# Kernel optimization log

Hardware: AMD Instinct MI355X
Metric: run time of the kernel (lower is better)

The kernel has to match this reference:

```python
import jax, jax.numpy as jnp
import numpy as np

N = 100000      # nodes
E = 1600000     # edges (before self-loops)
IN = 64         # in_channels
HID = 16        # hidden_channels
HEADS = 4       # num_heads
G = 512         # number of graphs in batch
SLOPE = 0.2     # GATConv leaky_relu negative_slope


def setup_inputs() -> dict:
    key = jax.random.key(0)
    ks = jax.random.split(key, 12)
    s = 0.1
    x = jax.random.normal(ks[0], (N, IN), jnp.float32)
    edge_index = jax.random.randint(ks[1], (2, E), 0, N, dtype=jnp.int64)
    batch = jnp.sort(jax.random.randint(ks[2], (N,), 0, G, dtype=jnp.int64))
    W1 = jax.random.normal(ks[3], (IN, HEADS * HID), jnp.float32) * s
    a1_src = jax.random.normal(ks[4], (HEADS, HID), jnp.float32) * s
    a1_dst = jax.random.normal(ks[5], (HEADS, HID), jnp.float32) * s
    b1 = jnp.zeros((HEADS * HID,), jnp.float32)
    W2 = jax.random.normal(ks[6], (HEADS * HID, HID), jnp.float32) * s
    a2_src = jax.random.normal(ks[7], (1, HID), jnp.float32) * s
    a2_dst = jax.random.normal(ks[8], (1, HID), jnp.float32) * s
    b2 = jnp.zeros((HID,), jnp.float32)
    Wc = jax.random.normal(ks[9], (HID, 1), jnp.float32) * s
    bc = jnp.zeros((1,), jnp.float32)
    return dict(x=x, edge_index=edge_index, batch=batch, W1=W1, a1_src=a1_src,
                a1_dst=a1_dst, b1=b1, W2=W2, a2_src=a2_src, a2_dst=a2_dst,
                b2=b2, Wc=Wc, bc=bc)


def gat_layer(x, src, dst, W, a_s, a_d, bias, heads, out_ch, concat):
    # PyG GATConv: linear -> per-edge attention logits -> segment softmax over dst -> scatter aggregate
    n = x.shape[0]
    h = (x @ W).reshape(n, heads, out_ch)              # [N, H, C]
    al_s = jnp.sum(h * a_s, axis=-1)                   # [N, H]
    al_d = jnp.sum(h * a_d, axis=-1)                   # [N, H]
    e = al_s[src] + al_d[dst]                          # [E, H]
    e = jnp.where(e > 0, e, SLOPE * e)                 # leaky_relu
    m = jax.ops.segment_max(e, dst, num_segments=n)    # per-dst max (self-loops ensure non-empty)
    p = jnp.exp(e - m[dst])
    denom = jax.ops.segment_sum(p, dst, num_segments=n)
    alpha = p / (denom[dst] + 1e-16)                   # [E, H]
    out = jax.ops.segment_sum(h[src] * alpha[:, :, None], dst, num_segments=n)  # [N, H, C]
    out = out.reshape(n, heads * out_ch) if concat else out.mean(axis=1)
    return out + bias


def reference(x, edge_index, batch, W1, a1_src, a1_dst, b1, W2, a2_src, a2_dst, b2, Wc, bc):
    loops = jnp.arange(N, dtype=edge_index.dtype)      # GATConv add_self_loops=True
    src = jnp.concatenate([edge_index[0], loops])
    dst = jnp.concatenate([edge_index[1], loops])
    h = jax.nn.elu(gat_layer(x, src, dst, W1, a1_src, a1_dst, b1, HEADS, HID, True))
    # dropout inactive (eval mode)
    h = jax.nn.elu(gat_layer(h, src, dst, W2, a2_src, a2_dst, b2, 1, HID, False))
    counts = jax.ops.segment_sum(jnp.ones((N,), h.dtype), batch, num_segments=G)
    pooled = jax.ops.segment_sum(h, batch, num_segments=G) / jnp.maximum(counts, 1.0)[:, None]
    return pooled @ Wc + bc
```

## Files before the change

### kernel.cpp

```cpp
#include <hip/hip_runtime.h>
#include <hip/hip_fp16.h>
#include <hip/hip_fp8.h>

#define N_NODES 100000
#define N_EDGES 1600000
#define ET      (N_EDGES + N_NODES)
#define NG      512
#define SLOPE   0.2f

#define BKT_SHIFT 9
#define NB_B   ((N_NODES + 511) / 512)
#define BCAP   10240
#define CHUNK_A 8192
#define NBLK_A ((ET + CHUNK_A - 1) / CHUNK_A)
#define H1B4   ((N_NODES + 1023) / 1024)

typedef _Float16 half8_t __attribute__((ext_vector_type(8)));
typedef float    f32x4_t __attribute__((ext_vector_type(4)));

__global__ __launch_bounds__(1024) void k_prepA(
    const float* __restrict__ x, const float* __restrict__ W1,
    const float* __restrict__ a1s, const float* __restrict__ a1d,
    const int* __restrict__ ei,
    int* __restrict__ gcnt, unsigned int* __restrict__ ebuf,
    __hip_fp8_e4m3* __restrict__ h1, float* __restrict__ al1s, float* __restrict__ al1d)
{
    __shared__ union U {
        struct { float Wl[64 * 64]; float asf[64]; float adf[64]; } p;
        struct { unsigned int stage[CHUNK_A]; unsigned char sbin[CHUNK_A];
                 int hist[NB_B]; int binst[NB_B]; int resv[NB_B]; int cur[NB_B];
                 int tmp[1024]; } a;
    } u;
    int tid = threadIdx.x;

    if (blockIdx.x < NBLK_A) {
        int base = blockIdx.x * CHUNK_A;
        int m = min(CHUNK_A, ET - base);
        for (int i = tid; i < NB_B; i += 1024) u.a.hist[i] = 0;
        __syncthreads();
        for (int i = tid; i < m; i += 1024) {
            int eid = base + i;
            int d = (eid < N_EDGES) ? ei[N_EDGES + eid] : (eid - N_EDGES);
            atomicAdd(&u.a.hist[d >> BKT_SHIFT], 1);
        }
        __syncthreads();
        int v = (tid < NB_B) ? u.a.hist[tid] : 0;
        u.a.tmp[tid] = v;
        __syncthreads();
        for (int off = 1; off < 1024; off <<= 1) {
            int t = (tid >= off) ? u.a.tmp[tid - off] : 0;
            __syncthreads();
            u.a.tmp[tid] += t;
            __syncthreads();
        }
        if (tid < NB_B) {
            int e = u.a.tmp[tid] - v;
            u.a.binst[tid] = e;
            u.a.cur[tid] = e;
            u.a.resv[tid] = v ? atomicAdd(&gcnt[tid], v) : 0;
        }
        __syncthreads();
        for (int i = tid; i < m; i += 1024) {
            int eid = base + i;
            int s, d;
            if (eid < N_EDGES) { s = ei[eid]; d = ei[N_EDGES + eid]; }
            else               { s = eid - N_EDGES; d = s; }
            int b = d >> BKT_SHIFT;
            int pos = atomicAdd(&u.a.cur[b], 1);
            u.a.stage[pos] = ((unsigned int)(d & 511) << 17) | (unsigned int)s;
            u.a.sbin[pos] = (unsigned char)b;
        }
        __syncthreads();
        for (int i = tid; i < m; i += 1024) {
            int b = u.a.sbin[i];
            ebuf[b * BCAP + u.a.resv[b] + (i - u.a.binst[b])] = u.a.stage[i];
        }
        return;
    }

    for (int i = tid; i < 64 * 64; i += 1024) u.p.Wl[i] = W1[i];
    if (tid < 64) { u.p.asf[tid] = a1s[tid]; u.p.adf[tid] = a1d[tid]; }
    __syncthreads();

    int wv = tid >> 6, lane = tid & 63;
    int m = lane & 15, q = lane >> 4;

    half8_t bf[4][2];
#pragma unroll
    for (int t = 0; t < 4; ++t)
#pragma unroll
        for (int s = 0; s < 2; ++s) {
            half8_t b;
#pragma unroll
            for (int j = 0; j < 8; ++j)
                b[j] = (_Float16)u.p.Wl[(s * 32 + q * 8 + j) * 64 + t * 16 + m];
            bf[t][s] = b;
        }

    int nodebase = (blockIdx.x - NBLK_A) * 1024 + wv * 64;
    for (int it = 0; it < 4; ++it) {
        int node0 = nodebase + it * 16;
        int node = node0 + m;
        half8_t av0 = {}, av1 = {};
        if (node < N_NODES) {
            const float4* xr = (const float4*)(x + (long long)node * 64);
            float4 p0 = xr[q * 2], p1 = xr[q * 2 + 1];
            float4 p2 = xr[q * 2 + 8], p3 = xr[q * 2 + 9];
            av0[0] = (_Float16)p0.x; av0[1] = (_Float16)p0.y;
            av0[2] = (_Float16)p0.z; av0[3] = (_Float16)p0.w;
            av0[4] = (_Float16)p1.x; av0[5] = (_Float16)p1.y;
            av0[6] = (_Float16)p1.z; av0[7] = (_Float16)p1.w;
            av1[0] = (_Float16)p2.x; av1[1] = (_Float16)p2.y;
            av1[2] = (_Float16)p2.z; av1[3] = (_Float16)p2.w;
            av1[4] = (_Float16)p3.x; av1[5] = (_Float16)p3.y;
            av1[6] = (_Float16)p3.z; av1[7] = (_Float16)p3.w;
        }
        f32x4_t acc[4] = {{0,0,0,0},{0,0,0,0},{0,0,0,0},{0,0,0,0}};
#pragma unroll
        for (int t = 0; t < 4; ++t) {
            acc[t] = __builtin_amdgcn_mfma_f32_16x16x32_f16(av0, bf[t][0], acc[t], 0, 0, 0);
            acc[t] = __builtin_amdgcn_mfma_f32_16x16x32_f16(av1, bf[t][1], acc[t], 0, 0, 0);
        }
#pragma unroll
        for (int r = 0; r < 4; ++r) {
            int nr = node0 + q * 4 + r;
            bool ok = nr < N_NODES;
#pragma unroll
            for (int t = 0; t < 4; ++t) {
                float v = acc[t][r];
                if (ok) h1[(long long)nr * 64 + t * 16 + m] = __hip_fp8_e4m3(v);
                float ps = v * u.p.asf[t * 16 + m];
                float pd = v * u.p.adf[t * 16 + m];
                ps += __shfl_xor(ps, 1); ps += __shfl_xor(ps, 2);
                ps += __shfl_xor(ps, 4); ps += __shfl_xor(ps, 8);
                pd += __shfl_xor(pd, 1); pd += __shfl_xor(pd, 2);
                pd += __shfl_xor(pd, 4); pd += __shfl_xor(pd, 8);
                if (ok && m == t) { al1s[nr * 4 + t] = ps; al1d[nr * 4 + t] = pd; }
            }
        }
    }
}

__global__ __launch_bounds__(1024) void k_passB(
    const unsigned int* __restrict__ ebuf, const int* __restrict__ gcnt,
    int* __restrict__ csr, int* __restrict__ offs, int* __restrict__ deg)
{
    __shared__ int ldeg[512];
    __shared__ int lofs[512];
    __shared__ int lcur[512];
    int tid = threadIdx.x;
    int b = blockIdx.x;
    int nb0 = b << BKT_SHIFT;
    int nn = min(512, N_NODES - nb0);
    int gbase = b * BCAP, cnt = gcnt[b];
    if (tid < 512) ldeg[tid] = 0;
    __syncthreads();
    for (int i = tid; i < cnt; i += 1024)
        atomicAdd(&ldeg[ebuf[gbase + i] >> 17], 1);
    __syncthreads();
    int v = 0;
    if (tid < 512) { v = ldeg[tid]; lofs[tid] = v; }
    __syncthreads();
    for (int off = 1; off < 512; off <<= 1) {
        int t = (tid >= off && tid < 512) ? lofs[tid - off] : 0;
        __syncthreads();
        if (tid < 512) lofs[tid] += t;
        __syncthreads();
    }
    if (tid < 512) {
        int e = lofs[tid] - v;
        lcur[tid] = e;
        if (tid < nn) { offs[nb0 + tid] = gbase + e; deg[nb0 + tid] = v; }
    }
    __syncthreads();
    for (int i = tid; i < cnt; i += 1024) {
        unsigned int ev = ebuf[gbase + i];
        int dl = ev >> 17, s = (int)(ev & 0x1FFFF);
        int p = atomicAdd(&lcur[dl], 1);
        csr[gbase + p] = s;
    }
}

__global__ __launch_bounds__(256) void k_agg1(
    const int* __restrict__ offs, const int* __restrict__ deg, const int* __restrict__ csr,
    const __hip_fp8_e4m3* __restrict__ h1, const float* __restrict__ al1s, const float* __restrict__ al1d,
    const float* __restrict__ b1, __half* __restrict__ h1bg)
{
    __shared__ int   sarr[4][64];
    __shared__ float warr[4][4 * 72];
    __shared__ __align__(16) float h1b[4][64];
    int tid = threadIdx.x;
    int wv = tid >> 6, lane = tid & 63;
    int eslot = lane >> 4;
    int cq = lane & 15;
    int h = cq >> 2;
    int cq4 = cq * 4;
    int node = blockIdx.x * 4 + wv;
    int st = offs[node], dg = deg[node];
    const float4 ald4 = *(const float4*)(al1d + node * 4);
    float b1l = b1[lane];
    const char* __restrict__ h1c = (const char*)h1;

    float a0 = 0.f, a1 = 0.f, a2 = 0.f, a3 = 0.f, den = 0.f;
    for (int base = 0; base < dg; base += 64) {
        int m = min(64, dg - base);
        int s = 0;
        float w0 = 0.f, w1 = 0.f, w2 = 0.f, w3 = 0.f;
        if (lane < m) {
            s = csr[st + base + lane];
            const float4 as4 = *(const float4*)(al1s + s * 4);
            float e0 = as4.x + ald4.x; e0 = e0 > 0.f ? e0 : SLOPE * e0;
            float e1 = as4.y + ald4.y; e1 = e1 > 0.f ? e1 : SLOPE * e1;
            float e2 = as4.z + ald4.z; e2 = e2 > 0.f ? e2 : SLOPE * e2;
            float e3 = as4.w + ald4.w; e3 = e3 > 0.f ? e3 : SLOPE * e3;
            w0 = __expf(e0); w1 = __expf(e1); w2 = __expf(e2); w3 = __expf(e3);
        }
        sarr[wv][lane] = s << 6;
        warr[wv][0 * 72 + lane] = w0;
        warr[wv][1 * 72 + lane] = w1;
        warr[wv][2 * 72 + lane] = w2;
        warr[wv][3 * 72 + lane] = w3;
        int m4 = (m + 3) & ~3;
#pragma unroll 4
        for (int j0 = 0; j0 < m4; j0 += 4) {
            int j = j0 + eslot;
            int off = sarr[wv][j] + cq4;
            float wgt = warr[wv][h * 72 + j];
            unsigned int pk = *(const unsigned int*)(h1c + off);
            a0 = fmaf(wgt, __builtin_amdgcn_cvt_f32_fp8(pk, 0), a0);
            a1 = fmaf(wgt, __builtin_amdgcn_cvt_f32_fp8(pk, 1), a1);
            a2 = fmaf(wgt, __builtin_amdgcn_cvt_f32_fp8(pk, 2), a2);
            a3 = fmaf(wgt, __builtin_amdgcn_cvt_f32_fp8(pk, 3), a3);
            den += wgt;
        }
    }
    a0 += __shfl_xor(a0, 16); a0 += __shfl_xor(a0, 32);
    a1 += __shfl_xor(a1, 16); a1 += __shfl_xor(a1, 32);
    a2 += __shfl_xor(a2, 16); a2 += __shfl_xor(a2, 32);
    a3 += __shfl_xor(a3, 16); a3 += __shfl_xor(a3, 32);
    den += __shfl_xor(den, 16); den += __shfl_xor(den, 32);
    if (lane < 16)
        *(float4*)&h1b[wv][cq4] = make_float4(a0, a1, a2, a3);
    float denc = __shfl(den, (lane >> 4) << 2);
    float v = h1b[wv][lane] / (denc + 1e-16f) + b1l;
    v = v > 0.f ? v : __expf(v) - 1.f;
    h1bg[(long long)node * 64 + lane] = __float2half_rn(v);
}

__global__ __launch_bounds__(256) void k_mid(
    const __half* __restrict__ h1bg, const float* __restrict__ W2,
    const float* __restrict__ a2s, const float* __restrict__ a2d,
    __half* __restrict__ h2, float* __restrict__ al2s, float* __restrict__ al2d)
{
    __shared__ float W2l[64 * 16];
    int tid = threadIdx.x;
    for (int i = tid; i < 64 * 16; i += 256) W2l[i] = W2[i];
    __syncthreads();
    int wv = tid >> 6, lane = tid & 63;
    int m = lane & 15, q = lane >> 4;
    half8_t bf[2];
#pragma unroll
    for (int s = 0; s < 2; ++s) {
        half8_t b;
#pragma unroll
        for (int j = 0; j < 8; ++j)
            b[j] = (_Float16)W2l[(s * 32 + q * 8 + j) * 16 + m];
        bf[s] = b;
    }
    int node0 = blockIdx.x * 64 + wv * 16;
    half8_t av0 = {}, av1 = {};
    if (node0 + m < N_NODES) {
        const __half* ar = h1bg + (long long)(node0 + m) * 64;
        av0 = *(const half8_t*)(ar + q * 8);
        av1 = *(const half8_t*)(ar + 32 + q * 8);
    }
    f32x4_t acc = {0, 0, 0, 0};
    acc = __builtin_amdgcn_mfma_f32_16x16x32_f16(av0, bf[0], acc, 0, 0, 0);
    acc = __builtin_amdgcn_mfma_f32_16x16x32_f16(av1, bf[1], acc, 0, 0, 0);
    float a2sm = a2s[m], a2dm = a2d[m];
#pragma unroll
    for (int r = 0; r < 4; ++r) {
        int nr = node0 + q * 4 + r;
        bool ok = nr < N_NODES;
        float v = acc[r];
        if (ok) h2[nr * 16 + m] = __float2half_rn(v);
        float ps = v * a2sm, pd = v * a2dm;
        ps += __shfl_xor(ps, 1); ps += __shfl_xor(ps, 2);
        ps += __shfl_xor(ps, 4); ps += __shfl_xor(ps, 8);
        pd += __shfl_xor(pd, 1); pd += __shfl_xor(pd, 2);
        pd += __shfl_xor(pd, 4); pd += __shfl_xor(pd, 8);
        if (ok && m == 0) { al2s[nr] = ps; al2d[nr] = pd; }
    }
}

__global__ __launch_bounds__(256) void k_agg2(
    const int* __restrict__ offs, const int* __restrict__ deg, const int* __restrict__ csr,
    const __half* __restrict__ h2, const float* __restrict__ al2s, const float* __restrict__ al2d,
    const float* __restrict__ b2, const int* __restrict__ batch, float* __restrict__ pooled)
{
    __shared__ int    sarr[4][64];
    __shared__ float  warr[4][64];
    __shared__ float2 pl[4][8];
    __shared__ int    gl[4];
    int tid = threadIdx.x;
    int wv = tid >> 6, lane = tid & 63;
    int ec = lane >> 3, cc = lane & 7;
    int node = blockIdx.x * 4 + wv;
    int st = offs[node], dg = deg[node];
    float ald = al2d[node];
    const __half2* __restrict__ h2v = (const __half2*)h2;

    float a0 = 0.f, a1 = 0.f, den = 0.f;
    for (int base = 0; base < dg; base += 64) {
        int m = min(64, dg - base);
        int s = 0; float wl = 0.f;
        if (lane < m) {
            s = csr[st + base + lane];
            float e = al2s[s] + ald;
            e = e > 0.f ? e : SLOPE * e;
            wl = __expf(e);
        }
        sarr[wv][lane] = s;
        warr[wv][lane] = wl;
        int m8 = (m + 7) & ~7;
#pragma unroll 2
        for (int j0 = 0; j0 < m8; j0 += 8) {
            int j = j0 + ec;
            int s2i = sarr[wv][j];
            float wgt = warr[wv][j];
            __half2 hv = h2v[s2i * 8 + cc];
            a0 = fmaf(__low2float(hv), wgt, a0);
            a1 = fmaf(__high2float(hv), wgt, a1);
            den += wgt;
        }
    }
    a0 += __shfl_xor(a0, 8);  a1 += __shfl_xor(a1, 8);  den += __shfl_xor(den, 8);
    a0 += __shfl_xor(a0, 16); a1 += __shfl_xor(a1, 16); den += __shfl_xor(den, 16);
    a0 += __shfl_xor(a0, 32); a1 += __shfl_xor(a1, 32); den += __shfl_xor(den, 32);
    if (lane < 8) {
        float inv = 1.f / (den + 1e-16f);
        float v0 = a0 * inv + b2[2 * cc];
        float v1 = a1 * inv + b2[2 * cc + 1];
        v0 = v0 > 0.f ? v0 : __expf(v0) - 1.f;
        v1 = v1 > 0.f ? v1 : __expf(v1) - 1.f;
        pl[wv][cc] = make_float2(v0, v1);
    }
    if (lane == 0) gl[wv] = batch[node];
    __syncthreads();
    if (wv == 0 && lane < 8) {
        int g0 = gl[0], g3 = gl[3];
        if (g0 == g3) {
            float2 s0 = pl[0][lane], s1 = pl[1][lane], s2 = pl[2][lane], s3 = pl[3][lane];
            atomicAdd(&pooled[g0 * 16 + 2 * lane],     s0.x + s1.x + s2.x + s3.x);
            atomicAdd(&pooled[g0 * 16 + 2 * lane + 1], s0.y + s1.y + s2.y + s3.y);
        } else {
#pragma unroll
            for (int nd = 0; nd < 4; ++nd) {
                float2 s = pl[nd][lane];
                atomicAdd(&pooled[gl[nd] * 16 + 2 * lane],     s.x);
                atomicAdd(&pooled[gl[nd] * 16 + 2 * lane + 1], s.y);
            }
        }
    }
}

__global__ __launch_bounds__(256) void k_cls(
    const float* __restrict__ pooled, const int* __restrict__ batch,
    const float* __restrict__ Wc, const float* __restrict__ bc, float* __restrict__ out)
{
    int g = blockIdx.x * 256 + threadIdx.x;
    if (g >= NG) return;
    int lo = 0, hi = N_NODES;
    while (lo < hi) { int mid = (lo + hi) >> 1; if (batch[mid] < g) lo = mid + 1; else hi = mid; }
    int s = lo;
    lo = 0; hi = N_NODES;
    while (lo < hi) { int mid = (lo + hi) >> 1; if (batch[mid] < g + 1) lo = mid + 1; else hi = mid; }
    float cnt = fmaxf((float)(lo - s), 1.0f);
    float acc = 0.f;
#pragma unroll
    for (int c = 0; c < 16; ++c) acc += pooled[g * 16 + c] * Wc[c];
    out[g] = acc / cnt + bc[0];
}

extern "C" void kernel_launch(void* const* d_in, const int* in_sizes, int n_in,
                              void* d_out, int out_size, void* d_ws, size_t ws_size,
                              hipStream_t stream)
{
    const float* x    = (const float*)d_in[0];
    const int*   ei   = (const int*)d_in[1];
    const int*   batc = (const int*)d_in[2];
    const float* W1   = (const float*)d_in[3];
    const float* a1s  = (const float*)d_in[4];
    const float* a1d  = (const float*)d_in[5];
    const float* b1   = (const float*)d_in[6];
    const float* W2   = (const float*)d_in[7];
    const float* a2s  = (const float*)d_in[8];
    const float* a2d  = (const float*)d_in[9];
    const float* b2   = (const float*)d_in[10];
    const float* Wc   = (const float*)d_in[11];
    const float* bc   = (const float*)d_in[12];
    float* out = (float*)d_out;

    char* ws = (char*)d_ws;
    size_t off = 0;
    auto carveB = [&](size_t bytes) {
        void* p = ws + off;
        off += ((bytes + 15) & ~(size_t)15);
        return p;
    };
    auto carve = [&](size_t elems) { return carveB(elems * 4); };
    int*   gcnt   = (int*)  carve(NB_B);
    float* pooled = (float*)carve((size_t)NG * 16);
    size_t zero_bytes = off;
    unsigned int* ebuf = (unsigned int*)carve((size_t)NB_B * BCAP);
    int*   csr    = (int*)  carve((size_t)NB_B * BCAP);
    int*   offs   = (int*)  carve(N_NODES);
    int*   deg    = (int*)  carve(N_NODES);
    __hip_fp8_e4m3* h1 = (__hip_fp8_e4m3*)carveB((size_t)N_NODES * 64);
    float* al1s   = (float*)carve((size_t)N_NODES * 4);
    float* al1d   = (float*)carve((size_t)N_NODES * 4);
    __half* h1bg  = (__half*)carveB((size_t)N_NODES * 64 * 2);
    __half* h2    = (__half*)carveB((size_t)N_NODES * 16 * 2);
    float* al2s   = (float*)carve(N_NODES);
    float* al2d   = (float*)carve(N_NODES);

    hipMemsetAsync(d_ws, 0, zero_bytes, stream);

    k_prepA<<<NBLK_A + H1B4, 1024, 0, stream>>>(x, W1, a1s, a1d, ei, gcnt, ebuf, h1, al1s, al1d);
    k_passB<<<NB_B, 1024, 0, stream>>>(ebuf, gcnt, csr, offs, deg);
    k_agg1 <<<N_NODES / 4, 256, 0, stream>>>(offs, deg, csr, h1, al1s, al1d, b1, h1bg);
    k_mid  <<<(N_NODES + 63) / 64, 256, 0, stream>>>(h1bg, W2, a2s, a2d, h2, al2s, al2d);
    k_agg2 <<<N_NODES / 4, 256, 0, stream>>>(offs, deg, csr, h2, al2s, al2d, b2, batc, pooled);
    k_cls  <<<NG / 256, 256, 0, stream>>>(pooled, batc, Wc, bc, out);
}
```

Before: 269.1 us.

## Precompute per-edge attention weights in CSR order before aggregation kernels

Per-edge exp(leaky_relu) attention weights for layer 1 are now computed inside the CSR scatter pass and stored as float4 in CSR order. Layer 2 gets a new edge-parallel kernel that writes its weights to a float array. The aggregation kernels then read contiguous weights instead of gathering al_s[src] randomly inside the latency-bound per-node loop. The cost is extra writes and reads of about 27 MB for layer 1 and 7 MB for layer 2, one more kernel launch, and random al1s gathers moved into passB.

```diff
diff --git a/kernel.cpp b/kernel.cpp
--- a/kernel.cpp
+++ b/kernel.cpp
@@ -143,7 +143,9 @@
 
 __global__ __launch_bounds__(1024) void k_passB(
     const unsigned int* __restrict__ ebuf, const int* __restrict__ gcnt,
-    int* __restrict__ csr, int* __restrict__ offs, int* __restrict__ deg)
+    const float* __restrict__ al1s, const float* __restrict__ al1d,
+    int* __restrict__ csr, float4* __restrict__ w1q,
+    int* __restrict__ offs, int* __restrict__ deg)
 {
     __shared__ int ldeg[512];
     __shared__ int lofs[512];
@@ -173,17 +175,26 @@
         if (tid < nn) { offs[nb0 + tid] = gbase + e; deg[nb0 + tid] = v; }
     }
     __syncthreads();
+    const float4* __restrict__ as4p = (const float4*)al1s;
+    const float4* __restrict__ ad4p = (const float4*)al1d;
     for (int i = tid; i < cnt; i += 1024) {
         unsigned int ev = ebuf[gbase + i];
-        int dl = ev >> 17, s = (int)(ev & 0x1FFFF);
+        int dl = (int)(ev >> 17), s = (int)(ev & 0x1FFFF);
         int p = atomicAdd(&lcur[dl], 1);
-        csr[gbase + p] = s;
+        csr[gbase + p] = (int)ev;
+        float4 as4 = as4p[s];
+        float4 ad4 = ad4p[nb0 + dl];
+        float e0 = as4.x + ad4.x; e0 = e0 > 0.f ? e0 : SLOPE * e0;
+        float e1 = as4.y + ad4.y; e1 = e1 > 0.f ? e1 : SLOPE * e1;
+        float e2 = as4.z + ad4.z; e2 = e2 > 0.f ? e2 : SLOPE * e2;
+        float e3 = as4.w + ad4.w; e3 = e3 > 0.f ? e3 : SLOPE * e3;
+        w1q[gbase + p] = make_float4(__expf(e0), __expf(e1), __expf(e2), __expf(e3));
     }
 }
 
 __global__ __launch_bounds__(256) void k_agg1(
     const int* __restrict__ offs, const int* __restrict__ deg, const int* __restrict__ csr,
-    const __hip_fp8_e4m3* __restrict__ h1, const float* __restrict__ al1s, const float* __restrict__ al1d,
+    const float4* __restrict__ w1q, const __hip_fp8_e4m3* __restrict__ h1,
     const float* __restrict__ b1, __half* __restrict__ h1bg)
 {
     __shared__ int   sarr[4][64];
@@ -197,7 +208,6 @@
     int cq4 = cq * 4;
     int node = blockIdx.x * 4 + wv;
     int st = offs[node], dg = deg[node];
-    const float4 ald4 = *(const float4*)(al1d + node * 4);
     float b1l = b1[lane];
     const char* __restrict__ h1c = (const char*)h1;
 
@@ -207,13 +217,9 @@
         int s = 0;
         float w0 = 0.f, w1 = 0.f, w2 = 0.f, w3 = 0.f;
         if (lane < m) {
-            s = csr[st + base + lane];
-            const float4 as4 = *(const float4*)(al1s + s * 4);
-            float e0 = as4.x + ald4.x; e0 = e0 > 0.f ? e0 : SLOPE * e0;
-            float e1 = as4.y + ald4.y; e1 = e1 > 0.f ? e1 : SLOPE * e1;
-            float e2 = as4.z + ald4.z; e2 = e2 > 0.f ? e2 : SLOPE * e2;
-            float e3 = as4.w + ald4.w; e3 = e3 > 0.f ? e3 : SLOPE * e3;
-            w0 = __expf(e0); w1 = __expf(e1); w2 = __expf(e2); w3 = __expf(e3);
+            s = csr[st + base + lane] & 0x1FFFF;
+            float4 w4 = w1q[st + base + lane];
+            w0 = w4.x; w1 = w4.y; w2 = w4.z; w3 = w4.w;
         }
         sarr[wv][lane] = s << 6;
         warr[wv][0 * 72 + lane] = w0;
@@ -293,9 +299,25 @@
     }
 }
 
+__global__ __launch_bounds__(256) void k_ew2(
+    const int* __restrict__ csr, const int* __restrict__ gcnt,
+    const float* __restrict__ al2s, const float* __restrict__ al2d,
+    float* __restrict__ w2q)
+{
+    int b = blockIdx.x / (BCAP / 256);
+    int p = (blockIdx.x % (BCAP / 256)) * 256 + threadIdx.x;
+    if (p >= gcnt[b]) return;
+    unsigned int e = (unsigned int)csr[b * BCAP + p];
+    int s = (int)(e & 0x1FFFF);
+    int node = (b << BKT_SHIFT) + (int)(e >> 17);
+    float v = al2s[s] + al2d[node];
+    v = v > 0.f ? v : SLOPE * v;
+    w2q[b * BCAP + p] = __expf(v);
+}
+
 __global__ __launch_bounds__(256) void k_agg2(
     const int* __restrict__ offs, const int* __restrict__ deg, const int* __restrict__ csr,
-    const __half* __restrict__ h2, const float* __restrict__ al2s, const float* __restrict__ al2d,
+    const float* __restrict__ w2q, const __half* __restrict__ h2,
     const float* __restrict__ b2, const int* __restrict__ batch, float* __restrict__ pooled)
 {
     __shared__ int    sarr[4][64];
@@ -307,7 +329,6 @@
     int ec = lane >> 3, cc = lane & 7;
     int node = blockIdx.x * 4 + wv;
     int st = offs[node], dg = deg[node];
-    float ald = al2d[node];
     const __half2* __restrict__ h2v = (const __half2*)h2;
 
     float a0 = 0.f, a1 = 0.f, den = 0.f;
@@ -315,10 +336,8 @@
         int m = min(64, dg - base);
         int s = 0; float wl = 0.f;
         if (lane < m) {
-            s = csr[st + base + lane];
-            float e = al2s[s] + ald;
-            e = e > 0.f ? e : SLOPE * e;
-            wl = __expf(e);
+            s = csr[st + base + lane] & 0x1FFFF;
+            wl = w2q[st + base + lane];
         }
         sarr[wv][lane] = s;
         warr[wv][lane] = wl;
@@ -414,6 +433,8 @@
     size_t zero_bytes = off;
     unsigned int* ebuf = (unsigned int*)carve((size_t)NB_B * BCAP);
     int*   csr    = (int*)  carve((size_t)NB_B * BCAP);
+    float4* w1q   = (float4*)carveB((size_t)NB_B * BCAP * 16);
+    float* w2q    = (float*)carve((size_t)NB_B * BCAP);
     int*   offs   = (int*)  carve(N_NODES);
     int*   deg    = (int*)  carve(N_NODES);
     __hip_fp8_e4m3* h1 = (__hip_fp8_e4m3*)carveB((size_t)N_NODES * 64);
@@ -427,9 +448,10 @@
     hipMemsetAsync(d_ws, 0, zero_bytes, stream);
 
     k_prepA<<<NBLK_A + H1B4, 1024, 0, stream>>>(x, W1, a1s, a1d, ei, gcnt, ebuf, h1, al1s, al1d);
-    k_passB<<<NB_B, 1024, 0, stream>>>(ebuf, gcnt, csr, offs, deg);
-    k_agg1 <<<N_NODES / 4, 256, 0, stream>>>(offs, deg, csr, h1, al1s, al1d, b1, h1bg);
+    k_passB<<<NB_B, 1024, 0, stream>>>(ebuf, gcnt, al1s, al1d, csr, w1q, offs, deg);
+    k_agg1 <<<N_NODES / 4, 256, 0, stream>>>(offs, deg, csr, w1q, h1, b1, h1bg);
     k_mid  <<<(N_NODES + 63) / 64, 256, 0, stream>>>(h1bg, W2, a2s, a2d, h2, al2s, al2d);
-    k_agg2 <<<N_NODES / 4, 256, 0, stream>>>(offs, deg, csr, h2, al2s, al2d, b2, batc, pooled);
+    k_ew2  <<<NB_B * (BCAP / 256), 256, 0, stream>>>(csr, gcnt, al2s, al2d, w2q);
+    k_agg2 <<<N_NODES / 4, 256, 0, stream>>>(offs, deg, csr, w2q, h2, b2, batc, pooled);
     k_cls  <<<NG / 256, 256, 0, stream>>>(pooled, batc, Wc, bc, out);
 }
```

Result: slower. 296.4 us (+10.1%).

## Widen gather loads in aggregation kernels and replace atomic pooling with segmented pool

Applied to the files above, without the earlier changes.

In the layer-1 aggregation, each lane now gathers a full 16-byte fp8 head row, where it previously loaded 4 bytes, and converts it with packed fp8-to-f32 conversions. Each wave therefore covers 16 edges per iteration instead of 4. Layer-2 aggregation likewise loads 16 bytes of fp16 features per lane and writes per-node outputs to a buffer, no longer atomically adding into pooled sums. A new per-graph pool kernel then reduces the contiguous node ranges and applies the classifier. The change also adds bucket capacity guards, trading an extra 6.4MB buffer write/read and a longer shuffle reduction for fewer memory transactions and no atomics.

```diff
diff --git a/kernel.cpp b/kernel.cpp
--- a/kernel.cpp
+++ b/kernel.cpp
@@ -17,6 +17,7 @@
 
 typedef _Float16 half8_t __attribute__((ext_vector_type(8)));
 typedef float    f32x4_t __attribute__((ext_vector_type(4)));
+typedef float    f32x2_t __attribute__((ext_vector_type(2)));
 
 __global__ __launch_bounds__(1024) void k_prepA(
     const float* __restrict__ x, const float* __restrict__ W1,
@@ -73,7 +74,9 @@
         __syncthreads();
         for (int i = tid; i < m; i += 1024) {
             int b = u.a.sbin[i];
-            ebuf[b * BCAP + u.a.resv[b] + (i - u.a.binst[b])] = u.a.stage[i];
+            int dst = u.a.resv[b] + (i - u.a.binst[b]);
+            if (dst < BCAP)
+                ebuf[b * BCAP + dst] = u.a.stage[i];
         }
         return;
     }
@@ -152,7 +155,7 @@
     int b = blockIdx.x;
     int nb0 = b << BKT_SHIFT;
     int nn = min(512, N_NODES - nb0);
-    int gbase = b * BCAP, cnt = gcnt[b];
+    int gbase = b * BCAP, cnt = min(gcnt[b], BCAP);
     if (tid < 512) ldeg[tid] = 0;
     __syncthreads();
     for (int i = tid; i < cnt; i += 1024)
@@ -191,17 +194,16 @@
     __shared__ __align__(16) float h1b[4][64];
     int tid = threadIdx.x;
     int wv = tid >> 6, lane = tid & 63;
-    int eslot = lane >> 4;
-    int cq = lane & 15;
-    int h = cq >> 2;
-    int cq4 = cq * 4;
+    int es = lane >> 2;
+    int qd = lane & 3;
     int node = blockIdx.x * 4 + wv;
     int st = offs[node], dg = deg[node];
     const float4 ald4 = *(const float4*)(al1d + node * 4);
     float b1l = b1[lane];
     const char* __restrict__ h1c = (const char*)h1;
 
-    float a0 = 0.f, a1 = 0.f, a2 = 0.f, a3 = 0.f, den = 0.f;
+    f32x2_t acc[8] = {{0,0},{0,0},{0,0},{0,0},{0,0},{0,0},{0,0},{0,0}};
+    float den = 0.f;
     for (int base = 0; base < dg; base += 64) {
         int m = min(64, dg - base);
         int s = 0;
@@ -220,28 +222,42 @@
         warr[wv][1 * 72 + lane] = w1;
         warr[wv][2 * 72 + lane] = w2;
         warr[wv][3 * 72 + lane] = w3;
-        int m4 = (m + 3) & ~3;
-#pragma unroll 4
-        for (int j0 = 0; j0 < m4; j0 += 4) {
-            int j = j0 + eslot;
-            int off = sarr[wv][j] + cq4;
-            float wgt = warr[wv][h * 72 + j];
-            unsigned int pk = *(const unsigned int*)(h1c + off);
-            a0 = fmaf(wgt, __builtin_amdgcn_cvt_f32_fp8(pk, 0), a0);
-            a1 = fmaf(wgt, __builtin_amdgcn_cvt_f32_fp8(pk, 1), a1);
-            a2 = fmaf(wgt, __builtin_amdgcn_cvt_f32_fp8(pk, 2), a2);
-            a3 = fmaf(wgt, __builtin_amdgcn_cvt_f32_fp8(pk, 3), a3);
+        int m16 = (m + 15) & ~15;
+#pragma unroll 2
+        for (int j0 = 0; j0 < m16; j0 += 16) {
+            int j = j0 + es;
+            int off = sarr[wv][j] + qd * 16;
+            float wgt = warr[wv][qd * 72 + j];
+            uint4 r = *(const uint4*)(h1c + off);
+            f32x2_t wg2 = {wgt, wgt};
+            unsigned int dw[4] = {r.x, r.y, r.z, r.w};
+#pragma unroll
+            for (int k = 0; k < 4; ++k) {
+                acc[2 * k]     = __builtin_elementwise_fma(wg2,
+                    __builtin_amdgcn_cvt_pk_f32_fp8((int)dw[k], false), acc[2 * k]);
+                acc[2 * k + 1] = __builtin_elementwise_fma(wg2,
+                    __builtin_amdgcn_cvt_pk_f32_fp8((int)dw[k], true),  acc[2 * k + 1]);
+            }
             den += wgt;
         }
     }
-    a0 += __shfl_xor(a0, 16); a0 += __shfl_xor(a0, 32);
-    a1 += __shfl_xor(a1, 16); a1 += __shfl_xor(a1, 32);
-    a2 += __shfl_xor(a2, 16); a2 += __shfl_xor(a2, 32);
-    a3 += __shfl_xor(a3, 16); a3 += __shfl_xor(a3, 32);
-    den += __shfl_xor(den, 16); den += __shfl_xor(den, 32);
-    if (lane < 16)
-        *(float4*)&h1b[wv][cq4] = make_float4(a0, a1, a2, a3);
-    float denc = __shfl(den, (lane >> 4) << 2);
+#pragma unroll
+    for (int x = 4; x <= 32; x <<= 1) {
+#pragma unroll
+        for (int k = 0; k < 8; ++k) {
+            acc[k].x += __shfl_xor(acc[k].x, x);
+            acc[k].y += __shfl_xor(acc[k].y, x);
+        }
+        den += __shfl_xor(den, x);
+    }
+    if (lane < 4) {
+        int c0 = lane * 16;
+        *(float4*)&h1b[wv][c0 + 0]  = make_float4(acc[0].x, acc[0].y, acc[1].x, acc[1].y);
+        *(float4*)&h1b[wv][c0 + 4]  = make_float4(acc[2].x, acc[2].y, acc[3].x, acc[3].y);
+        *(float4*)&h1b[wv][c0 + 8]  = make_float4(acc[4].x, acc[4].y, acc[5].x, acc[5].y);
+        *(float4*)&h1b[wv][c0 + 12] = make_float4(acc[6].x, acc[6].y, acc[7].x, acc[7].y);
+    }
+    float denc = __shfl(den, lane >> 4);
     float v = h1b[wv][lane] / (denc + 1e-16f) + b1l;
     v = v > 0.f ? v : __expf(v) - 1.f;
     h1bg[(long long)node * 64 + lane] = __float2half_rn(v);
@@ -296,21 +312,22 @@
 __global__ __launch_bounds__(256) void k_agg2(
     const int* __restrict__ offs, const int* __restrict__ deg, const int* __restrict__ csr,
     const __half* __restrict__ h2, const float* __restrict__ al2s, const float* __restrict__ al2d,
-    const float* __restrict__ b2, const int* __restrict__ batch, float* __restrict__ pooled)
-{
-    __shared__ int    sarr[4][64];
-    __shared__ float  warr[4][64];
-    __shared__ float2 pl[4][8];
-    __shared__ int    gl[4];
+    const float* __restrict__ b2, float* __restrict__ hout)
+{
+    __shared__ int   sarr[4][64];
+    __shared__ float warr[4][64];
+    __shared__ __align__(16) float h2b[4][16];
     int tid = threadIdx.x;
     int wv = tid >> 6, lane = tid & 63;
-    int ec = lane >> 3, cc = lane & 7;
+    int es = lane >> 1;
+    int hf = lane & 1;
     int node = blockIdx.x * 4 + wv;
     int st = offs[node], dg = deg[node];
     float ald = al2d[node];
-    const __half2* __restrict__ h2v = (const __half2*)h2;
-
-    float a0 = 0.f, a1 = 0.f, den = 0.f;
+    const char* __restrict__ h2c = (const char*)h2;
+
+    f32x2_t acc[4] = {{0,0},{0,0},{0,0},{0,0}};
+    float den = 0.f;
     for (int base = 0; base < dg; base += 64) {
         int m = min(64, dg - base);
         int s = 0; float wl = 0.f;
@@ -320,66 +337,81 @@
             e = e > 0.f ? e : SLOPE * e;
             wl = __expf(e);
         }
-        sarr[wv][lane] = s;
+        sarr[wv][lane] = s << 5;
         warr[wv][lane] = wl;
-        int m8 = (m + 7) & ~7;
+        int m32 = (m + 31) & ~31;
 #pragma unroll 2
-        for (int j0 = 0; j0 < m8; j0 += 8) {
-            int j = j0 + ec;
-            int s2i = sarr[wv][j];
+        for (int j0 = 0; j0 < m32; j0 += 32) {
+            int j = j0 + es;
+            int off = sarr[wv][j] + hf * 16;
             float wgt = warr[wv][j];
-            __half2 hv = h2v[s2i * 8 + cc];
-            a0 = fmaf(__low2float(hv), wgt, a0);
-            a1 = fmaf(__high2float(hv), wgt, a1);
-            den += wgt;
-        }
-    }
-    a0 += __shfl_xor(a0, 8);  a1 += __shfl_xor(a1, 8);  den += __shfl_xor(den, 8);
-    a0 += __shfl_xor(a0, 16); a1 += __shfl_xor(a1, 16); den += __shfl_xor(den, 16);
-    a0 += __shfl_xor(a0, 32); a1 += __shfl_xor(a1, 32); den += __shfl_xor(den, 32);
+            uint4 r = *(const uint4*)(h2c + off);
+            unsigned int dw[4] = {r.x, r.y, r.z, r.w};
+#pragma unroll
+            for (int k = 0; k < 4; ++k) {
+                __half2 hv = *(__half2*)&dw[k];
+                acc[k].x = fmaf(__low2float(hv),  wgt, acc[k].x);
+                acc[k].y = fmaf(__high2float(hv), wgt, acc[k].y);
+            }
+            if (!hf) den += wgt;
+        }
+    }
+#pragma unroll
+    for (int x = 2; x <= 32; x <<= 1) {
+#pragma unroll
+        for (int k = 0; k < 4; ++k) {
+            acc[k].x += __shfl_xor(acc[k].x, x);
+            acc[k].y += __shfl_xor(acc[k].y, x);
+        }
+        den += __shfl_xor(den, x);
+    }
+    den = __shfl(den, 0);
+    if (lane < 2) {
+        int c0 = lane * 8;
+        *(float4*)&h2b[wv][c0 + 0] = make_float4(acc[0].x, acc[0].y, acc[1].x, acc[1].y);
+        *(float4*)&h2b[wv][c0 + 4] = make_float4(acc[2].x, acc[2].y, acc[3].x, acc[3].y);
+    }
     if (lane < 8) {
         float inv = 1.f / (den + 1e-16f);
-        float v0 = a0 * inv + b2[2 * cc];
-        float v1 = a1 * inv + b2[2 * cc + 1];
+        float v0 = h2b[wv][2 * lane]     * inv + b2[2 * lane];
+        float v1 = h2b[wv][2 * lane + 1] * inv + b2[2 * lane + 1];
         v0 = v0 > 0.f ? v0 : __expf(v0) - 1.f;
         v1 = v1 > 0.f ? v1 : __expf(v1) - 1.f;
-        pl[wv][cc] = make_float2(v0, v1);
-    }
-    if (lane == 0) gl[wv] = batch[node];
-    __syncthreads();
-    if (wv == 0 && lane < 8) {
-        int g0 = gl[0], g3 = gl[3];
-        if (g0 == g3) {
-            float2 s0 = pl[0][lane], s1 = pl[1][lane], s2 = pl[2][lane], s3 = pl[3][lane];
-            atomicAdd(&pooled[g0 * 16 + 2 * lane],     s0.x + s1.x + s2.x + s3.x);
-            atomicAdd(&pooled[g0 * 16 + 2 * lane + 1], s0.y + s1.y + s2.y + s3.y);
-        } else {
-#pragma unroll
-            for (int nd = 0; nd < 4; ++nd) {
-                float2 s = pl[nd][lane];
-                atomicAdd(&pooled[gl[nd] * 16 + 2 * lane],     s.x);
-                atomicAdd(&pooled[gl[nd] * 16 + 2 * lane + 1], s.y);
-            }
-        }
-    }
-}
-
-__global__ __launch_bounds__(256) void k_cls(
-    const float* __restrict__ pooled, const int* __restrict__ batch,
+        ((float2*)hout)[node * 8 + lane] = make_float2(v0, v1);
+    }
+}
+
+__global__ __launch_bounds__(256) void k_pool(
+    const float* __restrict__ hout, const int* __restrict__ batch,
     const float* __restrict__ Wc, const float* __restrict__ bc, float* __restrict__ out)
 {
-    int g = blockIdx.x * 256 + threadIdx.x;
-    if (g >= NG) return;
-    int lo = 0, hi = N_NODES;
-    while (lo < hi) { int mid = (lo + hi) >> 1; if (batch[mid] < g) lo = mid + 1; else hi = mid; }
-    int s = lo;
-    lo = 0; hi = N_NODES;
-    while (lo < hi) { int mid = (lo + hi) >> 1; if (batch[mid] < g + 1) lo = mid + 1; else hi = mid; }
-    float cnt = fmaxf((float)(lo - s), 1.0f);
-    float acc = 0.f;
-#pragma unroll
-    for (int c = 0; c < 16; ++c) acc += pooled[g * 16 + c] * Wc[c];
-    out[g] = acc / cnt + bc[0];
+    __shared__ float red[16][17];
+    __shared__ int bnd[2];
+    int g = blockIdx.x;
+    int t = threadIdx.x, c = t & 15, slot = t >> 4;
+    if (t < 2) {
+        int key = g + t;
+        int lo = 0, hi = N_NODES;
+        while (lo < hi) { int mid = (lo + hi) >> 1; if (batch[mid] < key) lo = mid + 1; else hi = mid; }
+        bnd[t] = lo;
+    }
+    __syncthreads();
+    int s = bnd[0], e = bnd[1];
+    float sum = 0.f;
+    for (int n = s + slot; n < e; n += 16)
+        sum += hout[n * 16 + c];
+    red[slot][c] = sum;
+    __syncthreads();
+    if (t < 16) {
+        float tot = 0.f;
+#pragma unroll
+        for (int k = 0; k < 16; ++k) tot += red[k][t];
+        float cnt = fmaxf((float)(e - s), 1.0f);
+        float pc = (tot / cnt) * Wc[t];
+        pc += __shfl_xor(pc, 1); pc += __shfl_xor(pc, 2);
+        pc += __shfl_xor(pc, 4); pc += __shfl_xor(pc, 8);
+        if (t == 0) out[g] = pc + bc[0];
+    }
 }
 
 extern "C" void kernel_launch(void* const* d_in, const int* in_sizes, int n_in,
@@ -410,7 +442,6 @@
     };
     auto carve = [&](size_t elems) { return carveB(elems * 4); };
     int*   gcnt   = (int*)  carve(NB_B);
-    float* pooled = (float*)carve((size_t)NG * 16);
     size_t zero_bytes = off;
     unsigned int* ebuf = (unsigned int*)carve((size_t)NB_B * BCAP);
     int*   csr    = (int*)  carve((size_t)NB_B * BCAP);
@@ -423,6 +454,7 @@
     __half* h2    = (__half*)carveB((size_t)N_NODES * 16 * 2);
     float* al2s   = (float*)carve(N_NODES);
     float* al2d   = (float*)carve(N_NODES);
+    float* hout   = (float*)carve((size_t)N_NODES * 16);
 
     hipMemsetAsync(d_ws, 0, zero_bytes, stream);
 
@@ -430,6 +462,6 @@
     k_passB<<<NB_B, 1024, 0, stream>>>(ebuf, gcnt, csr, offs, deg);
     k_agg1 <<<N_NODES / 4, 256, 0, stream>>>(offs, deg, csr, h1, al1s, al1d, b1, h1bg);
     k_mid  <<<(N_NODES + 63) / 64, 256, 0, stream>>>(h1bg, W2, a2s, a2d, h2, al2s, al2d);
-    k_agg2 <<<N_NODES / 4, 256, 0, stream>>>(offs, deg, csr, h2, al2s, al2d, b2, batc, pooled);
-    k_cls  <<<NG / 256, 256, 0, stream>>>(pooled, batc, Wc, bc, out);
-}
+    k_agg2 <<<N_NODES / 4, 256, 0, stream>>>(offs, deg, csr, h2, al2s, al2d, b2, hout);
+    k_pool <<<NG, 256, 0, stream>>>(hout, batc, Wc, bc, out);
+}
```

After: 308.5 us. 14.6% more time.
